# Kernel optimization log

Hardware: AMD Instinct MI355X
Metric: run time of the kernel (lower is better)

The kernel has to match this reference:

```python
import jax, jax.numpy as jnp
import numpy as np

B, D, T, K = 32768, 1024, 100, 4  # batch, input_dim, num_trees, 2**(tree_depth-1)

def setup_inputs() -> dict:
    key = jax.random.key(0)
    k1, k2, k3, k4, k5 = jax.random.split(key, 5)
    s1 = 1.0 / np.sqrt(D)
    s2 = 1.0 / np.sqrt(K)
    return {
        "x": jax.random.normal(k1, (B, D), dtype=jnp.float32),
        "W1": jax.random.uniform(k2, (T, K, D), jnp.float32, -s1, s1),  # per-tree first Linear
        "b1": jax.random.uniform(k3, (T, K), jnp.float32, -s1, s1),
        "final_weight": jnp.full((T,), 1.0 / T, dtype=jnp.float32),
        "fc_w": jax.random.uniform(k4, (2, K), jnp.float32, -s2, s2),
        "fc_b": jax.random.uniform(k5, (2,), jnp.float32, -s2, s2),
    }

def reference(x, W1, b1, final_weight, fc_w, fc_b):
    # split_probs for all trees at once: [B, T, K]
    split = jnp.einsum("bd,tkd->btk", x, W1) + b1[None, :, :]
    leaf = jax.nn.sigmoid(split)  # tree[1] is Sigmoid applied to split_probs
    # sum(split.unsqueeze(1)*leaf.unsqueeze(2), -1) == leaf * sum_k(split)
    tree_out = leaf * jnp.sum(split, axis=-1, keepdims=True)  # [B, T, K]
    weighted = jnp.einsum("btk,t->bk", tree_out, final_weight)  # [B, K]
    logits = weighted @ fc_w.T + fc_b  # [B, 2]
    return logits
```

## Files before the change

### kernel.cpp

```cpp
#include <hip/hip_runtime.h>
#include <hip/hip_bf16.h>


typedef __bf16 bf16x8 __attribute__((ext_vector_type(8)));
typedef float f32x4 __attribute__((ext_vector_type(4)));

#define B_ROWS 32768
#define D_DIM  1024
#define N_COLS 400
#define NPAD   448
#define BM     128
#define BK     32
#define NCHUNK 32
#define NSLOT  4
#define THREADS 512
#define NTPW 7
#define MT   4

__device__ __forceinline__ unsigned short f2bf(float f) {
    unsigned int u = __float_as_uint(f);
    u += 0x7FFFu + ((u >> 16) & 1u);
    return (unsigned short)(u >> 16);
}
__device__ __forceinline__ unsigned int pk2(float a, float b) {
    return (unsigned int)f2bf(a) | ((unsigned int)f2bf(b) << 16);
}
__device__ __forceinline__ uint4 cvt8u(float4 a, float4 b) {
    uint4 u;
    u.x = pk2(a.x, a.y); u.y = pk2(a.z, a.w);
    u.z = pk2(b.x, b.y); u.w = pk2(b.z, b.w);
    return u;
}
__device__ __forceinline__ bf16x8 cvt8(float4 a, float4 b) {
    return __builtin_bit_cast(bf16x8, cvt8u(a, b));
}

__global__ void cvt_pad_bf16_kernel(const float* __restrict__ in,
                                    unsigned short* __restrict__ out) {
    size_t i = ((size_t)blockIdx.x * 256 + threadIdx.x) * 8;
    if (i < (size_t)N_COLS * D_DIM) {
        float4 v0 = *reinterpret_cast<const float4*>(in + i);
        float4 v1 = *reinterpret_cast<const float4*>(in + i + 4);
        *reinterpret_cast<uint4*>(out + i) = cvt8u(v0, v1);
    } else {
        uint4 z; z.x = z.y = z.z = z.w = 0u;
        *reinterpret_cast<uint4*>(out + i) = z;
    }
}

__device__ __forceinline__ void gl_lds16(const unsigned short* g,
                                         unsigned short* l) {
    __builtin_amdgcn_global_load_lds(
        (const __attribute__((address_space(1))) unsigned int*)g,
        (__attribute__((address_space(3))) unsigned int*)l,
        16, 0, 0);
}

#define FOR_N_(OP, m) OP(m,0) OP(m,1) OP(m,2) OP(m,3) OP(m,4) OP(m,5) OP(m,6)
#define FOR_MN(OP) FOR_N_(OP,0) FOR_N_(OP,1) FOR_N_(OP,2) FOR_N_(OP,3)

#define DECL_ACC(m,n) f32x4 acc##m##n = {};
#define MFMA_MN(m,n) acc##m##n = __builtin_amdgcn_mfma_f32_16x16x32_bf16( \
        afr##m, bfr##n, acc##m##n, 0, 0, 0);

template <int MODE>
__global__ __launch_bounds__(THREADS, 2) void xgb_v18(
    const float* __restrict__ x,
    const void*  __restrict__ b_any,
    const float* __restrict__ b1,
    const float* __restrict__ fw,
    const float* __restrict__ fcw,
    const float* __restrict__ fcb,
    float* __restrict__ out)
{
    __shared__ __align__(16) unsigned short Aslot[NSLOT][BM * BK];
    __shared__ __align__(16) unsigned short Bslot[NSLOT][NPAD * BK];
    __shared__ float Pbuf[BM * 4 * 2];

    const int tid  = threadIdx.x;
    const int wave = tid >> 6;
    const int lane = tid & 63;
    const int quad = lane >> 4;
    const int l15  = lane & 15;
    const int mh   = wave >> 2;
    const int nf   = wave & 3;
    const int row0 = blockIdx.x * BM;

    FOR_MN(DECL_ACC)

    if (MODE == 0) {
        const unsigned short* w1b = (const unsigned short*)b_any;

#define BDECL(t) const unsigned short* bsrc##t; int bdst##t; \
        { const int s_ = wave + 7 * (t); \
          const int rb_ = s_ * 16 + (lane >> 2); \
          const int cc_ = ((lane & 3) - (rb_ >> 1)) & 3; \
          bsrc##t = w1b + (size_t)rb_ * D_DIM + cc_ * 8; \
          bdst##t = s_ * 512; }
        BDECL(0) BDECL(1) BDECL(2) BDECL(3)

#define STAGEB(kc, Bb) do { if (wave < 7) { \
        gl_lds16(bsrc0 + (kc), (Bb) + bdst0); \
        gl_lds16(bsrc1 + (kc), (Bb) + bdst1); \
        gl_lds16(bsrc2 + (kc), (Bb) + bdst2); \
        gl_lds16(bsrc3 + (kc), (Bb) + bdst3); } } while (0)

        const int r0a = tid >> 2, c0a = tid & 3;
        const float* asrc = x + (size_t)(row0 + r0a) * D_DIM + c0a * 8;
        const int adst = r0a * 32 + ((c0a + (r0a >> 1)) & 3) * 8;
        float4 aR0a, aR0b, aR1a, aR1b, aR2a, aR2b, aR3a, aR3b;

#define LOADA(S, kc) do { \
        aR##S##a = *reinterpret_cast<const float4*>(asrc + (kc));     \
        aR##S##b = *reinterpret_cast<const float4*>(asrc + (kc) + 4); } while (0)
#define WRITEA(S, Ab) do { \
        *reinterpret_cast<uint4*>((Ab) + adst) = cvt8u(aR##S##a, aR##S##b); \
        } while (0)

#define LOAD_AFR(m) { const int row_ = mh * 64 + (m) * 16 + l15; \
        const int p_ = (quad + (row_ >> 1)) & 3; \
        afr##m = *reinterpret_cast<const bf16x8*>(Ab_ + row_ * 32 + p_ * 8); }
#define LOAD_BFR(n) { const int row_ = (nf * NTPW + (n)) * 16 + l15; \
        const int p_ = (quad + (row_ >> 1)) & 3; \
        bfr##n = *reinterpret_cast<const bf16x8*>(Bb_ + row_ * 32 + p_ * 8); }

#define COMPUTE(PH) do { \
        const unsigned short* Ab_ = Aslot[PH]; \
        const unsigned short* Bb_ = Bslot[PH]; \
        bf16x8 afr0, afr1, afr2, afr3; \
        bf16x8 bfr0, bfr1, bfr2, bfr3, bfr4, bfr5, bfr6; \
        LOAD_AFR(0) LOAD_AFR(1) LOAD_AFR(2) LOAD_AFR(3) \
        LOAD_BFR(0) LOAD_BFR(1) LOAD_BFR(2) LOAD_BFR(3) \
        LOAD_BFR(4) LOAD_BFR(5) LOAD_BFR(6) \
        FOR_MN(MFMA_MN) \
        } while (0)

#define VMWAIT(c_) do { \
        if ((c_) <= NCHUNK - 3) { \
            if (wave < 7) asm volatile("s_waitcnt vmcnt(12)" ::: "memory"); \
            else          asm volatile("s_waitcnt vmcnt(4)"  ::: "memory"); \
        } else if ((c_) == NCHUNK - 2) { \
            if (wave < 7) asm volatile("s_waitcnt vmcnt(6)" ::: "memory"); \
            else          asm volatile("s_waitcnt vmcnt(2)" ::: "memory"); \
        } else { \
            asm volatile("s_waitcnt vmcnt(0)" ::: "memory"); \
        } \
        __builtin_amdgcn_sched_barrier(0); \
        } while (0)

#define CHUNK_BODY(PH, PH3, cc) do { \
        const int c_ = (cc) + (PH); \
        VMWAIT(c_); \
        WRITEA(PH, Aslot[PH]); \
        asm volatile("s_waitcnt lgkmcnt(0)" ::: "memory"); \
        __builtin_amdgcn_s_barrier(); \
        __builtin_amdgcn_sched_barrier(0); \
        if (c_ + 3 < NCHUNK) { \
            const int kc3_ = (c_ + 3) * BK; \
            STAGEB(kc3_, Bslot[PH3]); \
            LOADA(PH3, kc3_); \
        } \
        __builtin_amdgcn_sched_barrier(0); \
        COMPUTE(PH); \
        } while (0)

        STAGEB(0, Bslot[0]);  LOADA(0, 0);
        __builtin_amdgcn_sched_barrier(0);
        STAGEB(BK, Bslot[1]); LOADA(1, BK);
        __builtin_amdgcn_sched_barrier(0);
        STAGEB(2 * BK, Bslot[2]); LOADA(2, 2 * BK);
        __builtin_amdgcn_sched_barrier(0);

        #pragma unroll 1
        for (int cc = 0; cc < NCHUNK; cc += 4) {
            CHUNK_BODY(0, 3, cc);
            CHUNK_BODY(1, 0, cc);
            CHUNK_BODY(2, 1, cc);
            CHUNK_BODY(3, 2, cc);
        }
    } else {
        const float* af = x + (size_t)(row0 + mh * 64 + l15) * D_DIM + quad * 8;
#define PBF(n) const float* pbf##n; { \
        int r_ = (nf * NTPW + (n)) * 16 + l15; if (r_ > N_COLS - 1) r_ = 0; \
        pbf##n = (const float*)b_any + (size_t)r_ * D_DIM + quad * 8; }
        PBF(0) PBF(1) PBF(2) PBF(3) PBF(4) PBF(5) PBF(6)
        for (int step = 0; step < 32; ++step) {
            const int off = step * 32;
            bf16x8 afr0, afr1, afr2, afr3;
            bf16x8 bfr0, bfr1, bfr2, bfr3, bfr4, bfr5, bfr6;
#define LAF2(m) afr##m = cvt8( \
            *reinterpret_cast<const float4*>(af + (size_t)(m) * 16 * D_DIM + off), \
            *reinterpret_cast<const float4*>(af + (size_t)(m) * 16 * D_DIM + off + 4));
#define LBF2(n) bfr##n = cvt8( \
            *reinterpret_cast<const float4*>(pbf##n + off), \
            *reinterpret_cast<const float4*>(pbf##n + off + 4));
            LAF2(0) LAF2(1) LAF2(2) LAF2(3)
            LBF2(0) LBF2(1) LBF2(2) LBF2(3) LBF2(4) LBF2(5) LBF2(6)
            FOR_MN(MFMA_MN)
        }
    }

    const float fcw0 = fcw[l15 & 3];
    const float fcw1 = fcw[4 + (l15 & 3)];

#define PRE_N(n) \
    const int  col##n  = (nf * NTPW + (n)) * 16 + l15; \
    const bool ok##n   = (col##n < N_COLS); \
    const float bias##n = ok##n ? b1[ok##n ? col##n : 0] : 0.0f; \
    const float tw##n   = ok##n ? fw[ok##n ? (col##n >> 2) : 0] : 0.0f;
    PRE_N(0) PRE_N(1) PRE_N(2) PRE_N(3) PRE_N(4) PRE_N(5) PRE_N(6)

#define EPI_TERM(m,r,n) { \
        const float split_ = acc##m##n[r] + bias##n; \
        float s_ = split_; \
        s_ += __shfl_xor(s_, 1); \
        s_ += __shfl_xor(s_, 2); \
        const float leaf_ = 1.0f / (1.0f + __expf(-split_)); \
        const float val_ = tw##n * leaf_ * s_; \
        q0 += val_ * fcw0; q1 += val_ * fcw1; }

#define EPI_ONE(m,r) { \
        float q0 = 0.f, q1 = 0.f; \
        EPI_TERM(m,r,0) EPI_TERM(m,r,1) EPI_TERM(m,r,2) EPI_TERM(m,r,3) \
        EPI_TERM(m,r,4) EPI_TERM(m,r,5) EPI_TERM(m,r,6) \
        q0 += __shfl_xor(q0, 1); q0 += __shfl_xor(q0, 2); \
        q0 += __shfl_xor(q0, 4); q0 += __shfl_xor(q0, 8); \
        q1 += __shfl_xor(q1, 1); q1 += __shfl_xor(q1, 2); \
        q1 += __shfl_xor(q1, 4); q1 += __shfl_xor(q1, 8); \
        const int row_ = mh * 64 + (m) * 16 + quad * 4 + (r);    \
        if (l15 == 0) Pbuf[(row_ * 4 + nf) * 2 + 0] = q0; \
        if (l15 == 1) Pbuf[(row_ * 4 + nf) * 2 + 1] = q1; }

#define EPI_M(m) EPI_ONE(m,0) EPI_ONE(m,1) EPI_ONE(m,2) EPI_ONE(m,3)
    EPI_M(0) EPI_M(1) EPI_M(2) EPI_M(3)

    __syncthreads();

    if (tid < 2 * BM) {
        const int r = tid >> 1, j = tid & 1;
        float s = fcb[j];
        #pragma unroll
        for (int w = 0; w < 4; ++w)
            s += Pbuf[(r * 4 + w) * 2 + j];
        out[(size_t)(row0 + r) * 2 + j] = s;
    }
}

extern "C" void kernel_launch(void* const* d_in, const int* in_sizes, int n_in,
                              void* d_out, int out_size, void* d_ws, size_t ws_size,
                              hipStream_t stream) {
    const float* x   = (const float*)d_in[0];
    const float* W1  = (const float*)d_in[1];
    const float* b1  = (const float*)d_in[2];
    const float* fw  = (const float*)d_in[3];
    const float* fcw = (const float*)d_in[4];
    const float* fcb = (const float*)d_in[5];
    float* out = (float*)d_out;

    const size_t pad_elems = (size_t)NPAD * D_DIM;
    if (ws_size >= pad_elems * sizeof(unsigned short)) {
        unsigned short* w1b = (unsigned short*)d_ws;
        cvt_pad_bf16_kernel<<<(int)(pad_elems / 2048), 256, 0, stream>>>(W1, w1b);
        xgb_v18<0><<<B_ROWS / BM, THREADS, 0, stream>>>(
            x, (const void*)w1b, b1, fw, fcw, fcb, out);
    } else {
        xgb_v18<2><<<B_ROWS / BM, THREADS, 0, stream>>>(
            x, (const void*)W1, b1, fw, fcw, fcb, out);
    }
}
```

Baseline: 240.5 us.

## Load W1 fragments directly from global into registers, shrink tile to 64 rows

Replaces the 4-slot LDS staging of both A and B with a double-buffered LDS path for x only. The bf16 W1 fragments now go straight from global memory (L2-resident) into registers, prefetched one half-chunk ahead. The block shrinks to 64 rows and 4 waves with BK=64, which cuts LDS use so more blocks can be resident. The cost is that every block re-reads W1 from L2 per wave without LDS sharing, and there is less A reuse per block.

```diff
diff --git a/kernel.cpp b/kernel.cpp
--- a/kernel.cpp
+++ b/kernel.cpp
@@ -9,11 +9,10 @@
 #define D_DIM  1024
 #define N_COLS 400
 #define NPAD   448
-#define BM     128
-#define BK     32
-#define NCHUNK 32
-#define NSLOT  4
-#define THREADS 512
+#define BM     64
+#define BK     64
+#define NCHUNK 16
+#define THREADS 256
 #define NTPW 7
 #define MT   4
 
@@ -48,14 +47,6 @@
     }
 }
 
-__device__ __forceinline__ void gl_lds16(const unsigned short* g,
-                                         unsigned short* l) {
-    __builtin_amdgcn_global_load_lds(
-        (const __attribute__((address_space(1))) unsigned int*)g,
-        (__attribute__((address_space(3))) unsigned int*)l,
-        16, 0, 0);
-}
-
 #define FOR_N_(OP, m) OP(m,0) OP(m,1) OP(m,2) OP(m,3) OP(m,4) OP(m,5) OP(m,6)
 #define FOR_MN(OP) FOR_N_(OP,0) FOR_N_(OP,1) FOR_N_(OP,2) FOR_N_(OP,3)
 
@@ -64,7 +55,7 @@
         afr##m, bfr##n, acc##m##n, 0, 0, 0);
 
 template <int MODE>
-__global__ __launch_bounds__(THREADS, 2) void xgb_v18(
+__global__ __launch_bounds__(THREADS, 2) void xgb_v19(
     const float* __restrict__ x,
     const void*  __restrict__ b_any,
     const float* __restrict__ b1,
@@ -73,8 +64,7 @@
     const float* __restrict__ fcb,
     float* __restrict__ out)
 {
-    __shared__ __align__(16) unsigned short Aslot[NSLOT][BM * BK];
-    __shared__ __align__(16) unsigned short Bslot[NSLOT][NPAD * BK];
+    __shared__ __align__(16) unsigned short Abuf[2][BM * BK];
     __shared__ float Pbuf[BM * 4 * 2];
 
     const int tid  = threadIdx.x;
@@ -82,8 +72,7 @@
     const int lane = tid & 63;
     const int quad = lane >> 4;
     const int l15  = lane & 15;
-    const int mh   = wave >> 2;
-    const int nf   = wave & 3;
+    const int nf   = wave;
     const int row0 = blockIdx.x * BM;
 
     FOR_MN(DECL_ACC)
@@ -91,95 +80,86 @@
     if (MODE == 0) {
         const unsigned short* w1b = (const unsigned short*)b_any;
 
-#define BDECL(t) const unsigned short* bsrc##t; int bdst##t; \
-        { const int s_ = wave + 7 * (t); \
-          const int rb_ = s_ * 16 + (lane >> 2); \
-          const int cc_ = ((lane & 3) - (rb_ >> 1)) & 3; \
-          bsrc##t = w1b + (size_t)rb_ * D_DIM + cc_ * 8; \
-          bdst##t = s_ * 512; }
-        BDECL(0) BDECL(1) BDECL(2) BDECL(3)
-
-#define STAGEB(kc, Bb) do { if (wave < 7) { \
-        gl_lds16(bsrc0 + (kc), (Bb) + bdst0); \
-        gl_lds16(bsrc1 + (kc), (Bb) + bdst1); \
-        gl_lds16(bsrc2 + (kc), (Bb) + bdst2); \
-        gl_lds16(bsrc3 + (kc), (Bb) + bdst3); } } while (0)
-
-        const int r0a = tid >> 2, c0a = tid & 3;
-        const float* asrc = x + (size_t)(row0 + r0a) * D_DIM + c0a * 8;
-        const int adst = r0a * 32 + ((c0a + (r0a >> 1)) & 3) * 8;
-        float4 aR0a, aR0b, aR1a, aR1b, aR2a, aR2b, aR3a, aR3b;
+        const int r0a = tid >> 3, c0a = tid & 7;
+        const float* asrc0 = x + (size_t)(row0 + r0a) * D_DIM + c0a * 8;
+        const float* asrc1 = asrc0 + (size_t)32 * D_DIM;
+        const int adst0 = r0a * 64 + ((c0a + r0a) & 7) * 8;
+        float4 aRX0, aRX1, aRX2, aRX3;
+        float4 aRY0, aRY1, aRY2, aRY3;
 
 #define LOADA(S, kc) do { \
-        aR##S##a = *reinterpret_cast<const float4*>(asrc + (kc));     \
-        aR##S##b = *reinterpret_cast<const float4*>(asrc + (kc) + 4); } while (0)
+        aR##S##0 = *reinterpret_cast<const float4*>(asrc0 + (kc));     \
+        aR##S##1 = *reinterpret_cast<const float4*>(asrc0 + (kc) + 4); \
+        aR##S##2 = *reinterpret_cast<const float4*>(asrc1 + (kc));     \
+        aR##S##3 = *reinterpret_cast<const float4*>(asrc1 + (kc) + 4); } while (0)
 #define WRITEA(S, Ab) do { \
-        *reinterpret_cast<uint4*>((Ab) + adst) = cvt8u(aR##S##a, aR##S##b); \
+        *reinterpret_cast<uint4*>((Ab) + adst0)        = cvt8u(aR##S##0, aR##S##1); \
+        *reinterpret_cast<uint4*>((Ab) + adst0 + 2048) = cvt8u(aR##S##2, aR##S##3); \
         } while (0)
 
-#define LOAD_AFR(m) { const int row_ = mh * 64 + (m) * 16 + l15; \
-        const int p_ = (quad + (row_ >> 1)) & 3; \
-        afr##m = *reinterpret_cast<const bf16x8*>(Ab_ + row_ * 32 + p_ * 8); }
-#define LOAD_BFR(n) { const int row_ = (nf * NTPW + (n)) * 16 + l15; \
-        const int p_ = (quad + (row_ >> 1)) & 3; \
-        bfr##n = *reinterpret_cast<const bf16x8*>(Bb_ + row_ * 32 + p_ * 8); }
-
-#define COMPUTE(PH) do { \
-        const unsigned short* Ab_ = Aslot[PH]; \
-        const unsigned short* Bb_ = Bslot[PH]; \
+#define BPDECL(n) const unsigned short* pb##n = \
+        w1b + (size_t)((nf * NTPW + (n)) * 16 + l15) * D_DIM + quad * 8;
+        BPDECL(0) BPDECL(1) BPDECL(2) BPDECL(3) BPDECL(4) BPDECL(5) BPDECL(6)
+
+        uint4 bA0, bA1, bA2, bA3, bA4, bA5, bA6;
+        uint4 bB0, bB1, bB2, bB3, bB4, bB5, bB6;
+
+#define BLOAD(S, kc, h) do { \
+        b##S##0 = *reinterpret_cast<const uint4*>(pb0 + (kc) + (h) * 32); \
+        b##S##1 = *reinterpret_cast<const uint4*>(pb1 + (kc) + (h) * 32); \
+        b##S##2 = *reinterpret_cast<const uint4*>(pb2 + (kc) + (h) * 32); \
+        b##S##3 = *reinterpret_cast<const uint4*>(pb3 + (kc) + (h) * 32); \
+        b##S##4 = *reinterpret_cast<const uint4*>(pb4 + (kc) + (h) * 32); \
+        b##S##5 = *reinterpret_cast<const uint4*>(pb5 + (kc) + (h) * 32); \
+        b##S##6 = *reinterpret_cast<const uint4*>(pb6 + (kc) + (h) * 32); } while (0)
+
+#define LOAD_AFR(m, h) { const int row_ = (m) * 16 + l15; \
+        const int p_ = (quad + (h) * 4 + row_) & 7; \
+        afr##m = *reinterpret_cast<const bf16x8*>(Ab_ + row_ * 64 + p_ * 8); }
+
+#define COMPUTE_H(S, h) do { \
         bf16x8 afr0, afr1, afr2, afr3; \
-        bf16x8 bfr0, bfr1, bfr2, bfr3, bfr4, bfr5, bfr6; \
-        LOAD_AFR(0) LOAD_AFR(1) LOAD_AFR(2) LOAD_AFR(3) \
-        LOAD_BFR(0) LOAD_BFR(1) LOAD_BFR(2) LOAD_BFR(3) \
-        LOAD_BFR(4) LOAD_BFR(5) LOAD_BFR(6) \
+        LOAD_AFR(0, h) LOAD_AFR(1, h) LOAD_AFR(2, h) LOAD_AFR(3, h) \
+        bf16x8 bfr0 = __builtin_bit_cast(bf16x8, b##S##0); \
+        bf16x8 bfr1 = __builtin_bit_cast(bf16x8, b##S##1); \
+        bf16x8 bfr2 = __builtin_bit_cast(bf16x8, b##S##2); \
+        bf16x8 bfr3 = __builtin_bit_cast(bf16x8, b##S##3); \
+        bf16x8 bfr4 = __builtin_bit_cast(bf16x8, b##S##4); \
+        bf16x8 bfr5 = __builtin_bit_cast(bf16x8, b##S##5); \
+        bf16x8 bfr6 = __builtin_bit_cast(bf16x8, b##S##6); \
         FOR_MN(MFMA_MN) \
         } while (0)
 
-#define VMWAIT(c_) do { \
-        if ((c_) <= NCHUNK - 3) { \
-            if (wave < 7) asm volatile("s_waitcnt vmcnt(12)" ::: "memory"); \
-            else          asm volatile("s_waitcnt vmcnt(4)"  ::: "memory"); \
-        } else if ((c_) == NCHUNK - 2) { \
-            if (wave < 7) asm volatile("s_waitcnt vmcnt(6)" ::: "memory"); \
-            else          asm volatile("s_waitcnt vmcnt(2)" ::: "memory"); \
-        } else { \
-            asm volatile("s_waitcnt vmcnt(0)" ::: "memory"); \
-        } \
+#define CHUNK_BODY(PH, WS, LS, cc) do { \
+        const int c_ = (cc) + (PH); \
+        const int kc_ = c_ * BK; \
+        const unsigned short* Ab_ = Abuf[PH]; \
+        BLOAD(B, kc_, 1);                          \
+        COMPUTE_H(A, 0);                           \
+        if (c_ + 1 < NCHUNK) BLOAD(A, kc_ + BK, 0);  \
+        if (c_ + 2 < NCHUNK) LOADA(LS, kc_ + 2 * BK); \
+        COMPUTE_H(B, 1);                           \
+        if (c_ + 1 < NCHUNK) WRITEA(WS, Abuf[PH ^ 1]); \
+        asm volatile("s_waitcnt lgkmcnt(0)" ::: "memory"); \
         __builtin_amdgcn_sched_barrier(0); \
+        __builtin_amdgcn_s_barrier(); \
         } while (0)
 
-#define CHUNK_BODY(PH, PH3, cc) do { \
-        const int c_ = (cc) + (PH); \
-        VMWAIT(c_); \
-        WRITEA(PH, Aslot[PH]); \
-        asm volatile("s_waitcnt lgkmcnt(0)" ::: "memory"); \
-        __builtin_amdgcn_s_barrier(); \
-        __builtin_amdgcn_sched_barrier(0); \
-        if (c_ + 3 < NCHUNK) { \
-            const int kc3_ = (c_ + 3) * BK; \
-            STAGEB(kc3_, Bslot[PH3]); \
-            LOADA(PH3, kc3_); \
-        } \
-        __builtin_amdgcn_sched_barrier(0); \
-        COMPUTE(PH); \
-        } while (0)
-
-        STAGEB(0, Bslot[0]);  LOADA(0, 0);
+        LOADA(X, 0);
+        BLOAD(A, 0, 0);
+        WRITEA(X, Abuf[0]);
+        LOADA(Y, BK);
+        asm volatile("s_waitcnt lgkmcnt(0)" ::: "memory");
         __builtin_amdgcn_sched_barrier(0);
-        STAGEB(BK, Bslot[1]); LOADA(1, BK);
-        __builtin_amdgcn_sched_barrier(0);
-        STAGEB(2 * BK, Bslot[2]); LOADA(2, 2 * BK);
-        __builtin_amdgcn_sched_barrier(0);
+        __builtin_amdgcn_s_barrier();
 
         #pragma unroll 1
-        for (int cc = 0; cc < NCHUNK; cc += 4) {
-            CHUNK_BODY(0, 3, cc);
-            CHUNK_BODY(1, 0, cc);
-            CHUNK_BODY(2, 1, cc);
-            CHUNK_BODY(3, 2, cc);
+        for (int cc = 0; cc < NCHUNK; cc += 2) {
+            CHUNK_BODY(0, Y, X, cc);
+            CHUNK_BODY(1, X, Y, cc);
         }
     } else {
-        const float* af = x + (size_t)(row0 + mh * 64 + l15) * D_DIM + quad * 8;
+        const float* af = x + (size_t)(row0 + l15) * D_DIM + quad * 8;
 #define PBF(n) const float* pbf##n; { \
         int r_ = (nf * NTPW + (n)) * 16 + l15; if (r_ > N_COLS - 1) r_ = 0; \
         pbf##n = (const float*)b_any + (size_t)r_ * D_DIM + quad * 8; }
@@ -227,7 +207,7 @@
         q0 += __shfl_xor(q0, 4); q0 += __shfl_xor(q0, 8); \
         q1 += __shfl_xor(q1, 1); q1 += __shfl_xor(q1, 2); \
         q1 += __shfl_xor(q1, 4); q1 += __shfl_xor(q1, 8); \
-        const int row_ = mh * 64 + (m) * 16 + quad * 4 + (r);    \
+        const int row_ = (m) * 16 + quad * 4 + (r);            \
         if (l15 == 0) Pbuf[(row_ * 4 + nf) * 2 + 0] = q0; \
         if (l15 == 1) Pbuf[(row_ * 4 + nf) * 2 + 1] = q1; }
 
@@ -261,10 +241,10 @@
     if (ws_size >= pad_elems * sizeof(unsigned short)) {
         unsigned short* w1b = (unsigned short*)d_ws;
         cvt_pad_bf16_kernel<<<(int)(pad_elems / 2048), 256, 0, stream>>>(W1, w1b);
-        xgb_v18<0><<<B_ROWS / BM, THREADS, 0, stream>>>(
+        xgb_v19<0><<<B_ROWS / BM, THREADS, 0, stream>>>(
             x, (const void*)w1b, b1, fw, fcw, fcb, out);
     } else {
-        xgb_v18<2><<<B_ROWS / BM, THREADS, 0, stream>>>(
+        xgb_v19<2><<<B_ROWS / BM, THREADS, 0, stream>>>(
             x, (const void*)W1, b1, fw, fcw, fcb, out);
     }
 }
```

Result: slower. 317.8 us (+32.1%).
